# Optimization experiments

Measured on AMD Instinct MI355X. Metric: run time of the kernel, lower is better.

Reference implementation:

```python
import jax, jax.numpy as jnp
import numpy as np

B, S = 2, 1024
V, H = 32000, 1024
NH, NKV = 16, 8
HD = H // NH          # 64
L = 8
I = 4 * H             # 4096
EPS = 1e-6
THETA = 10000.0
NEG = -1e9


def setup_inputs() -> dict:
    key = jax.random.key(0)
    ks = jax.random.split(key, 12)
    std = 0.02
    f = lambda k, shape: jax.random.normal(k, shape, jnp.float32) * std
    return {
        "input_ids": jax.random.randint(ks[0], (B, S), 0, V, dtype=jnp.int32),
        "embed": f(ks[1], (V, H)),
        "Wq": f(ks[2], (L, H, NH * HD)),
        "Wk": f(ks[3], (L, H, NKV * HD)),
        "Wv": f(ks[4], (L, H, NKV * HD)),
        "Wo": f(ks[5], (L, NH * HD, H)),
        "Wg": f(ks[6], (L, H, I)),
        "Wu": f(ks[7], (L, H, I)),
        "Wd": f(ks[8], (L, I, H)),
        "ln1": jnp.ones((L, H), jnp.float32),
        "ln2": jnp.ones((L, H), jnp.float32),
        "norm_w": jnp.ones((H,), jnp.float32),
        "lm_head": f(ks[9], (H, V)),
    }


def _rmsnorm(x, w):
    var = jnp.mean(x * x, axis=-1, keepdims=True)
    return x * jax.lax.rsqrt(var + EPS) * w


def _rotate_half(x):
    x1, x2 = jnp.split(x, 2, axis=-1)
    return jnp.concatenate((-x2, x1), axis=-1)


def reference(input_ids, embed, Wq, Wk, Wv, Wo, Wg, Wu, Wd, ln1, ln2, norm_w, lm_head):
    # RoPE tables [S, HD] (freqs duplicated, matching cat((freqs, freqs)))
    inv_freq = 1.0 / (THETA ** (jnp.arange(0, HD, 2, dtype=jnp.float32) / HD))
    t = jnp.arange(S, dtype=jnp.float32)
    freqs = t[:, None] * inv_freq[None, :]
    emb = jnp.concatenate((freqs, freqs), axis=-1)
    cos = jnp.cos(emb)[None, None]  # [1,1,S,HD]
    sin = jnp.sin(emb)[None, None]
    # causal mask [S, S]
    mask = jnp.where(jnp.tril(jnp.ones((S, S), bool)), 0.0, NEG).astype(jnp.float32)

    def layer(h, p):
        wq, wk, wv, wo, wg, wu, wd, g1, g2 = p
        x = _rmsnorm(h, g1)
        q = (x @ wq).reshape(B, S, NH, HD).transpose(0, 2, 1, 3)   # [B,NH,S,HD]
        k = (x @ wk).reshape(B, S, NKV, HD).transpose(0, 2, 1, 3)  # [B,NKV,S,HD]
        v = (x @ wv).reshape(B, S, NKV, HD).transpose(0, 2, 1, 3)
        q = q * cos + _rotate_half(q) * sin
        k = k * cos + _rotate_half(k) * sin
        rep = NH // NKV
        k = jnp.repeat(k, rep, axis=1)  # GQA repeat_interleave
        v = jnp.repeat(v, rep, axis=1)
        scores = jnp.einsum("bhqd,bhkd->bhqk", q, k) / np.sqrt(HD) + mask
        probs = jax.nn.softmax(scores, axis=-1)
        o = jnp.einsum("bhqk,bhkd->bhqd", probs, v)
        o = o.transpose(0, 2, 1, 3).reshape(B, S, NH * HD)
        h = h + o @ wo
        x = _rmsnorm(h, g2)
        h = h + (jax.nn.silu(x @ wg) * (x @ wu)) @ wd
        return h, None

    h = embed[input_ids]  # [B,S,H]
    h, _ = jax.lax.scan(layer, h, (Wq, Wk, Wv, Wo, Wg, Wu, Wd, ln1, ln2))
    h = _rmsnorm(h, norm_w)
    return h @ lm_head  # logits [B,S,V]
```

## Files before the change

kernel.cpp:

```cpp
#include <hip/hip_runtime.h>


typedef unsigned short u16;
typedef __bf16  bf16x8 __attribute__((ext_vector_type(8)));
typedef unsigned short u16x8 __attribute__((ext_vector_type(8)));
typedef float   f32x4  __attribute__((ext_vector_type(4)));

#define DEV static __device__ __forceinline__

constexpr int NB  = 2;
constexpr int S   = 1024;
constexpr int NT  = NB * S;
constexpr int H   = 1024;
constexpr int NH  = 16;
constexpr int NKV = 8;
constexpr int HD  = 64;
constexpr int NL  = 8;
constexpr int FF  = 4096;
constexpr int V   = 32000;
constexpr int QKVW = 2048;

DEV float b2f(u16 x) { return __uint_as_float(((unsigned)x) << 16); }
DEV u16   f2b(float f) {
  unsigned i = __float_as_uint(f);
  return (u16)((i + 0x7fffu + ((i >> 16) & 1u)) >> 16);
}

DEV void gload16(const void* g, void* l) {
  __builtin_amdgcn_global_load_lds(
      (const __attribute__((address_space(1))) void*)g,
      (__attribute__((address_space(3))) void*)l, 16, 0, 0);
}

DEV bf16x8 ld128(const u16* p) { return *reinterpret_cast<const bf16x8*>(p); }

template <int N> DEV void waitvm() {
  if constexpr (N == 0)      asm volatile("s_waitcnt vmcnt(0)" ::: "memory");
  else if constexpr (N == 2) asm volatile("s_waitcnt vmcnt(2)" ::: "memory");
  else if constexpr (N == 3) asm volatile("s_waitcnt vmcnt(3)" ::: "memory");
  else if constexpr (N == 4) asm volatile("s_waitcnt vmcnt(4)" ::: "memory");
  else if constexpr (N == 6) asm volatile("s_waitcnt vmcnt(6)" ::: "memory");
  else                       asm volatile("s_waitcnt vmcnt(8)" ::: "memory");
}

template <int EPI>
__global__ __launch_bounds__(512, 2) void gemm256_k(
    const u16* __restrict__ A, int lda,
    const u16* __restrict__ Bt, int ldb,
    void* __restrict__ C, int ldc, int K)
{
  __shared__ __align__(16) u16 Asm[4][256 * 32];
  __shared__ __align__(16) u16 Bsm[4][256 * 32];

  const int tid  = threadIdx.x;
  const int lane = tid & 63;
  const int lrow = lane & 15;
  const int g    = lane >> 4;
  const int wid  = tid >> 6;
  const int wm   = wid >> 2, wn = wid & 3;

  int flat = blockIdx.y * gridDim.x + blockIdx.x;
  const int cpx = (gridDim.x * gridDim.y) >> 3;
  flat = (flat & 7) * cpx + (flat >> 3);
  const int bx = flat % gridDim.x;
  const int by = flat / gridDim.x;

  const int r0   = tid >> 2, pp = tid & 3;
  const int row1 = 128 + (tid >> 2);
  const int p0 = pp ^ ((r0 ^ (r0 >> 2)) & 3);
  const int p1 = pp ^ ((row1 ^ (row1 >> 2)) & 3);
  const u16* aS0 = A  + (size_t)(bx * 256 + r0)   * lda + p0 * 8;
  const u16* aS1 = A  + (size_t)(bx * 256 + row1) * lda + p1 * 8;
  const u16* bS0 = Bt + (size_t)(by * 256 + r0)   * ldb + p0 * 8;
  const u16* bS1 = Bt + (size_t)(by * 256 + row1) * ldb + p1 * 8;
  const int aB0 = tid * 16, aB1 = (512 + tid) * 16;

  int aOff[8], bOff[4];
  #pragma unroll
  for (int fm = 0; fm < 8; fm++) {
    const int r = wm * 128 + fm * 16 + lrow;
    aOff[fm] = r * 32 + (g ^ ((r ^ (r >> 2)) & 3)) * 8;
  }
  #pragma unroll
  for (int fn = 0; fn < 4; fn++) {
    const int r = wn * 64 + fn * 16 + lrow;
    bOff[fn] = r * 32 + (g ^ ((r ^ (r >> 2)) & 3)) * 8;
  }

  f32x4 acc[8][4] = {};
  const int ntk = K / 32;

  #pragma unroll
  for (int ts = 0; ts < 3; ts++) {
    const long kt = (long)ts * 32;
    gload16(aS0 + kt, (char*)Asm[ts] + aB0);
    gload16(bS0 + kt, (char*)Bsm[ts] + aB0);
    gload16(aS1 + kt, (char*)Asm[ts] + aB1);
    gload16(bS1 + kt, (char*)Bsm[ts] + aB1);
  }
  asm volatile("s_waitcnt vmcnt(8)" ::: "memory");
  __builtin_amdgcn_s_barrier();

#define KTILE(VMW, STG)                                                         \
  {                                                                             \
    const int rs = t & 3, ss = (t + 3) & 3;                                     \
    const long kt = (long)(t + 3) * 32;                                         \
    bf16x8 af[4], bf[4];                                                        \
    _Pragma("unroll") for (int i = 0; i < 4; i++) bf[i] = ld128(&Bsm[rs][bOff[i]]); \
    _Pragma("unroll") for (int i = 0; i < 4; i++) af[i] = ld128(&Asm[rs][aOff[i]]); \
    if (STG) { gload16(aS0 + kt, (char*)Asm[ss] + aB0);                         \
               gload16(bS0 + kt, (char*)Bsm[ss] + aB0); }                       \
    __builtin_amdgcn_s_barrier();                                               \
    asm volatile("s_waitcnt lgkmcnt(0)" ::: "memory");                          \
    __builtin_amdgcn_sched_barrier(0);                                          \
    __builtin_amdgcn_s_setprio(1);                                              \
    _Pragma("unroll") for (int m = 0; m < 4; m++)                               \
      _Pragma("unroll") for (int n = 0; n < 4; n++)                             \
        acc[m][n] = __builtin_amdgcn_mfma_f32_16x16x32_bf16(af[m], bf[n], acc[m][n], 0, 0, 0); \
    __builtin_amdgcn_s_setprio(0);                                              \
    __builtin_amdgcn_s_barrier();                                               \
    _Pragma("unroll") for (int i = 0; i < 4; i++) af[i] = ld128(&Asm[rs][aOff[4 + i]]); \
    if (STG) { gload16(aS1 + kt, (char*)Asm[ss] + aB1);                         \
               gload16(bS1 + kt, (char*)Bsm[ss] + aB1); }                       \
    __builtin_amdgcn_s_barrier();                                               \
    asm volatile("s_waitcnt lgkmcnt(0)" ::: "memory");                          \
    __builtin_amdgcn_sched_barrier(0);                                          \
    __builtin_amdgcn_s_setprio(1);                                              \
    _Pragma("unroll") for (int m = 0; m < 4; m++)                               \
      _Pragma("unroll") for (int n = 0; n < 4; n++)                             \
        acc[4 + m][n] = __builtin_amdgcn_mfma_f32_16x16x32_bf16(af[m], bf[n], acc[4 + m][n], 0, 0, 0); \
    __builtin_amdgcn_s_setprio(0);                                              \
    VMW;                                                                        \
    __builtin_amdgcn_sched_barrier(0);                                          \
    __builtin_amdgcn_s_barrier();                                               \
  }

  {
    int t = 0;
    for (; t < ntk - 3; ++t) KTILE(asm volatile("s_waitcnt vmcnt(8)" ::: "memory"), true);
    KTILE(asm volatile("s_waitcnt vmcnt(4)" ::: "memory"), false); ++t;
    KTILE(asm volatile("s_waitcnt vmcnt(0)" ::: "memory"), false); ++t;
    KTILE((void)0, false);
  }
#undef KTILE

  if (EPI == 2) {
    #pragma unroll
    for (int fm = 0; fm < 8; fm++) {
      #pragma unroll
      for (int fp = 0; fp < 2; fp++) {
        #pragma unroll
        for (int r = 0; r < 4; r++) {
          const size_t row = bx * 256 + wm * 128 + fm * 16 + g * 4 + r;
          const int nb = by * 256 + wn * 64 + fp * 32;
          const int oc = (nb >> 5) * 16 + lrow;
          const float gg = acc[fm][2 * fp][r];
          const float uu = acc[fm][2 * fp + 1][r];
          ((u16*)C)[row * ldc + oc] = f2b(gg / (1.f + __expf(-gg)) * uu);
        }
      }
    }
  } else {
    #pragma unroll
    for (int fm = 0; fm < 8; fm++) {
      #pragma unroll
      for (int fn = 0; fn < 4; fn++) {
        #pragma unroll
        for (int r = 0; r < 4; r++) {
          const size_t row = bx * 256 + wm * 128 + fm * 16 + g * 4 + r;
          const size_t col = by * 256 + wn * 64 + fn * 16 + lrow;
          ((float*)C)[row * ldc + col] = acc[fm][fn][r];
        }
      }
    }
  }
}

template <int BM, int BN, int WM, int WN, int EPI>
__global__ __launch_bounds__(256) void gemm_k(
    const u16* __restrict__ A, int lda,
    const u16* __restrict__ Bt, int ldb,
    void* __restrict__ C, int ldc,
    const float2* __restrict__ tab, int K)
{
  constexpr int LA = (BM * 4) / 256;
  constexpr int LB = (BN * 4) / 256;
  constexpr int LT = LA + LB;

  __shared__ __align__(16) u16 Asm[4][BM * 32];
  __shared__ __align__(16) u16 Bsm[4][BN * 32];

  const int tid  = threadIdx.x;
  const int lane = tid & 63;
  const int lrow = lane & 15;
  const int kb   = lane >> 4;
  const int w    = tid >> 6;
  const int wm   = w / WN, wn = w % WN;
  constexpr int WR = BM / WM, WC = BN / WN;
  constexpr int FM = WR / 16, FN = WC / 16;

  const u16* aS[LA];
  const u16* bS[LB];
  #pragma unroll
  for (int i = 0; i < LA; i++) {
    const int row = (i * 256 + tid) >> 2, pp = tid & 3;
    const int p = pp ^ ((row ^ (row >> 2)) & 3);
    aS[i] = A + (size_t)(blockIdx.x * BM + row) * lda + p * 8;
  }
  #pragma unroll
  for (int i = 0; i < LB; i++) {
    const int row = (i * 256 + tid) >> 2, pp = tid & 3;
    const int p = pp ^ ((row ^ (row >> 2)) & 3);
    bS[i] = Bt + (size_t)(blockIdx.y * BN + row) * ldb + p * 8;
  }

  int aOff[FM], bOff[FN];
  #pragma unroll
  for (int fm = 0; fm < FM; fm++) {
    const int r = wm * WR + fm * 16 + lrow;
    aOff[fm] = r * 32 + (kb ^ ((r ^ (r >> 2)) & 3)) * 8;
  }
  #pragma unroll
  for (int fn = 0; fn < FN; fn++) {
    const int r = wn * WC + fn * 16 + lrow;
    bOff[fn] = r * 32 + (kb ^ ((r ^ (r >> 2)) & 3)) * 8;
  }

  f32x4 acc[FM][FN] = {};
  const int ntk = K / 32;

  #pragma unroll
  for (int ts = 0; ts < 3; ts++) {
    #pragma unroll
    for (int i = 0; i < LA; i++)
      gload16(aS[i] + ts * 32, (char*)Asm[ts] + (i * 256 + tid) * 16);
    #pragma unroll
    for (int i = 0; i < LB; i++)
      gload16(bS[i] + ts * 32, (char*)Bsm[ts] + (i * 256 + tid) * 16);
  }
  waitvm<2 * LT>();
  __builtin_amdgcn_s_barrier();

#define SKTILE(VMW, STG)                                                        \
  {                                                                             \
    const int rs = t & 3, ss = (t + 3) & 3;                                     \
    const long kt = (long)(t + 3) * 32;                                         \
    bf16x8 af[FM], bf[FN];                                                      \
    _Pragma("unroll") for (int i = 0; i < FN; i++) bf[i] = ld128(&Bsm[rs][bOff[i]]); \
    _Pragma("unroll") for (int i = 0; i < FM; i++) af[i] = ld128(&Asm[rs][aOff[i]]); \
    if (STG) {                                                                  \
      _Pragma("unroll") for (int i = 0; i < LA; i++)                            \
        gload16(aS[i] + kt, (char*)Asm[ss] + (i * 256 + tid) * 16);             \
      _Pragma("unroll") for (int i = 0; i < LB; i++)                            \
        gload16(bS[i] + kt, (char*)Bsm[ss] + (i * 256 + tid) * 16);             \
    }                                                                           \
    __builtin_amdgcn_s_barrier();                                               \
    asm volatile("s_waitcnt lgkmcnt(0)" ::: "memory");                          \
    __builtin_amdgcn_sched_barrier(0);                                          \
    __builtin_amdgcn_s_setprio(1);                                              \
    _Pragma("unroll") for (int m = 0; m < FM; m++)                              \
      _Pragma("unroll") for (int n = 0; n < FN; n++)                            \
        acc[m][n] = __builtin_amdgcn_mfma_f32_16x16x32_bf16(af[m], bf[n], acc[m][n], 0, 0, 0); \
    __builtin_amdgcn_s_setprio(0);                                              \
    VMW;                                                                        \
    __builtin_amdgcn_sched_barrier(0);                                          \
    __builtin_amdgcn_s_barrier();                                               \
  }

  {
    int t = 0;
    for (; t < ntk - 3; ++t) SKTILE(waitvm<2 * LT>(), true);
    SKTILE(waitvm<LT>(), false); ++t;
    SKTILE(waitvm<0>(), false); ++t;
    SKTILE((void)0, false);
  }
#undef SKTILE

  if (EPI == 4) {
    const int colb = blockIdx.y * BN + wn * WC;
    const int head = colb >> 6;
    const float qs = (head < 16) ? 0.125f : 1.0f;
    #pragma unroll
    for (int fm = 0; fm < FM; fm++) {
      #pragma unroll
      for (int r = 0; r < 4; r++) {
        const int row = blockIdx.x * BM + wm * WR + fm * 16 + kb * 4 + r;
        if (head >= 24) {
          #pragma unroll
          for (int fn = 0; fn < FN; fn++)
            ((u16*)C)[row * ldc + colb + fn * 16 + lrow] = f2b(acc[fm][fn][r]);
        } else {
          const int s = row & (S - 1);
          #pragma unroll
          for (int fp = 0; fp < 2; fp++) {
            const int d = fp * 16 + lrow;
            const float2 cs = tab[s * 32 + d];
            const float x1 = acc[fm][fp][r];
            const float x2 = acc[fm][fp + 2][r];
            ((u16*)C)[row * ldc + colb + d]      = f2b((x1 * cs.x - x2 * cs.y) * qs);
            ((u16*)C)[row * ldc + colb + d + 32] = f2b((x2 * cs.x + x1 * cs.y) * qs);
          }
        }
      }
    }
  } else {
    #pragma unroll
    for (int fm = 0; fm < FM; fm++) {
      #pragma unroll
      for (int fn = 0; fn < FN; fn++) {
        #pragma unroll
        for (int r = 0; r < 4; r++) {
          const int row = blockIdx.x * BM + wm * WR + fm * 16 + kb * 4 + r;
          const int col = blockIdx.y * BN + wn * WC + fn * 16 + lrow;
          ((u16*)C)[row * ldc + col] = f2b(acc[fm][fn][r]);
        }
      }
    }
  }
}

__global__ __launch_bounds__(256) void transpose_k(
    const float* __restrict__ W, u16* __restrict__ WT, int K, int N, int rmode,
    size_t wstride, size_t tstride)
{
  __shared__ float t[32][33];
  const float* Wp = W + (size_t)blockIdx.z * wstride;
  u16* WTp = WT + (size_t)blockIdx.z * tstride;
  const int k0 = blockIdx.x * 32, n0 = blockIdx.y * 32;
  const int tx = threadIdx.x & 31, ty = threadIdx.x >> 5;
  #pragma unroll
  for (int i = 0; i < 32; i += 8)
    t[ty + i][tx] = Wp[(size_t)(k0 + ty + i) * N + (n0 + tx)];
  __syncthreads();
  #pragma unroll
  for (int i = 0; i < 32; i += 8) {
    const int n = n0 + ty + i;
    const int orow = (rmode == 0) ? n : ((n >> 4) * 32 + (n & 15) + ((rmode == 2) ? 16 : 0));
    WTp[(size_t)orow * K + (k0 + tx)] = f2b(t[tx][ty + i]);
  }
}

__global__ __launch_bounds__(256) void embed_k(
    const int* __restrict__ ids, const float* __restrict__ E, float* __restrict__ h)
{
  const int t = blockIdx.x;
  const int id = ids[t];
  ((float4*)(h + t * H))[threadIdx.x] = ((const float4*)(E + (size_t)id * H))[threadIdx.x];
}

__global__ __launch_bounds__(256) void rmsnorm_k(
    const float* __restrict__ h, const float* __restrict__ w, u16* __restrict__ x)
{
  const int row = blockIdx.x;
  const float4 hv = ((const float4*)(h + row * H))[threadIdx.x];
  float s = hv.x * hv.x + hv.y * hv.y + hv.z * hv.z + hv.w * hv.w;
  #pragma unroll
  for (int off = 32; off; off >>= 1) s += __shfl_xor(s, off, 64);
  __shared__ float red[4];
  if ((threadIdx.x & 63) == 0) red[threadIdx.x >> 6] = s;
  __syncthreads();
  s = red[0] + red[1] + red[2] + red[3];
  const float scale = rsqrtf(s * (1.f / H) + 1e-6f);
  const float4 wv = ((const float4*)w)[threadIdx.x];
  ushort4 ov;
  ov.x = f2b(hv.x * scale * wv.x);
  ov.y = f2b(hv.y * scale * wv.y);
  ov.z = f2b(hv.z * scale * wv.z);
  ov.w = f2b(hv.w * scale * wv.w);
  ((ushort4*)(x + row * H))[threadIdx.x] = ov;
}

__global__ __launch_bounds__(256) void addnorm_k(
    float* __restrict__ h, const u16* __restrict__ dl,
    const float* __restrict__ w, u16* __restrict__ x)
{
  const int row = blockIdx.x;
  float4 hv = ((const float4*)(h + row * H))[threadIdx.x];
  const ushort4 dv = ((const ushort4*)(dl + row * H))[threadIdx.x];
  hv.x += b2f(dv.x); hv.y += b2f(dv.y); hv.z += b2f(dv.z); hv.w += b2f(dv.w);
  ((float4*)(h + row * H))[threadIdx.x] = hv;
  float s = hv.x * hv.x + hv.y * hv.y + hv.z * hv.z + hv.w * hv.w;
  #pragma unroll
  for (int off = 32; off; off >>= 1) s += __shfl_xor(s, off, 64);
  __shared__ float red[4];
  if ((threadIdx.x & 63) == 0) red[threadIdx.x >> 6] = s;
  __syncthreads();
  s = red[0] + red[1] + red[2] + red[3];
  const float scale = rsqrtf(s * (1.f / H) + 1e-6f);
  const float4 wv = ((const float4*)w)[threadIdx.x];
  ushort4 ov;
  ov.x = f2b(hv.x * scale * wv.x);
  ov.y = f2b(hv.y * scale * wv.y);
  ov.z = f2b(hv.z * scale * wv.z);
  ov.w = f2b(hv.w * scale * wv.w);
  ((ushort4*)(x + row * H))[threadIdx.x] = ov;
}

__global__ __launch_bounds__(256) void ropetab_k(float2* __restrict__ tab)
{
  const int idx = blockIdx.x * 256 + threadIdx.x;
  const int s = idx >> 5, d = idx & 31;
  const float ang = s * powf(10000.f, -(2.f * d) / 64.f);
  float sn, cs;
  sincosf(ang, &sn, &cs);
  tab[idx] = make_float2(cs, sn);
}

__global__ __launch_bounds__(256) void fattn_k(
    const u16* __restrict__ qkv, u16* __restrict__ o)
{
  __shared__ __align__(16) u16 Ks[64 * 64];
  __shared__ __align__(16) u16 Vt[64 * 72];
  __shared__ __align__(16) u16 Pw[4][16 * 64];

  const int tid  = threadIdx.x;
  const int lane = tid & 63;
  const int lrow = lane & 15;
  const int g    = lane >> 4;
  const int w    = tid >> 6;

  const int bid = blockIdx.x;
  const int j   = bid >> 3;
  const int bh  = (bid & 7) * 4 + (j & 3);
  const int bx  = 15 - (j >> 2);
  const int b = bh >> 4, hh = bh & 15, kh = hh >> 1;
  const int q0 = bx * 64;

  bf16x8 aq[2];
  {
    const int qrow = q0 + w * 16 + lrow;
    const u16* qp = qkv + (size_t)(b * S + qrow) * QKVW + hh * 64 + g * 8;
    aq[0] = *reinterpret_cast<const bf16x8*>(qp);
    aq[1] = *reinterpret_cast<const bf16x8*>(qp + 32);
  }

  f32x4 oacc[4] = {};
  float mrow[4], lsum[4];
  #pragma unroll
  for (int r = 0; r < 4; r++) { mrow[r] = -1e30f; lsum[r] = 0.f; }

  const int nt = bx + 1;
  for (int t = 0; t < nt; t++) {
    const int kv0 = t * 64;
    __syncthreads();

    #pragma unroll
    for (int i = 0; i < 2; i++) {
      const int c = i * 256 + tid;
      const int r = c >> 3, p = c & 7;
      gload16(qkv + (size_t)(b * S + kv0 + r) * QKVW + 1024 + kh * 64 + ((p ^ (r & 7)) * 8),
              (char*)Ks + c * 16);
    }
    u16x8 vreg[2];
    #pragma unroll
    for (int i = 0; i < 2; i++) {
      const int c = i * 256 + tid;
      const int k = c >> 3, dch = c & 7;
      vreg[i] = *reinterpret_cast<const u16x8*>(
          qkv + (size_t)(b * S + kv0 + k) * QKVW + 1536 + kh * 64 + dch * 8);
    }
    #pragma unroll
    for (int i = 0; i < 2; i++) {
      const int c = i * 256 + tid;
      const int k = c >> 3, d0 = (c & 7) * 8;
      #pragma unroll
      for (int j2 = 0; j2 < 8; j2++) {
        const int d = d0 + j2;
        Vt[d * 72 + (((k >> 3) ^ (d >> 3)) * 8) + (k & 7)] = vreg[i][j2];
      }
    }
    __syncthreads();

    f32x4 sacc[4] = {};
    #pragma unroll
    for (int n = 0; n < 4; n++) {
      const int row = n * 16 + lrow;
      #pragma unroll
      for (int k2 = 0; k2 < 2; k2++) {
        const bf16x8 bk = *reinterpret_cast<const bf16x8*>(
            Ks + row * 64 + (((k2 * 4 + g) ^ (row & 7)) * 8));
        sacc[n] = __builtin_amdgcn_mfma_f32_16x16x32_bf16(aq[k2], bk, sacc[n], 0, 0, 0);
      }
    }

    float rmv[4];
    #pragma unroll
    for (int r = 0; r < 4; r++) {
      const int qglob = q0 + w * 16 + g * 4 + r;
      float rm = -1e30f;
      #pragma unroll
      for (int n = 0; n < 4; n++) {
        const int kg = kv0 + n * 16 + lrow;
        if (kg > qglob) sacc[n][r] = -1e30f;
        rm = fmaxf(rm, sacc[n][r]);
      }
      #pragma unroll
      for (int mk = 1; mk < 16; mk <<= 1) rm = fmaxf(rm, __shfl_xor(rm, mk, 64));
      rmv[r] = rm;
    }

    int need = 0;
    #pragma unroll
    for (int r = 0; r < 4; r++) need |= (rmv[r] > mrow[r] + 8.f) ? 1 : 0;
    if (__any(need)) {
      #pragma unroll
      for (int r = 0; r < 4; r++) {
        const float mnew  = fmaxf(mrow[r], rmv[r]);
        const float scale = __expf(mrow[r] - mnew);
        mrow[r] = mnew;
        lsum[r] *= scale;
        #pragma unroll
        for (int dt = 0; dt < 4; dt++) oacc[dt][r] *= scale;
      }
    }

    #pragma unroll
    for (int r = 0; r < 4; r++) {
      float rs = 0.f;
      u16 pb[4];
      #pragma unroll
      for (int n = 0; n < 4; n++) {
        const float p = __expf(sacc[n][r] - mrow[r]);
        rs += p;
        pb[n] = f2b(p);
      }
      #pragma unroll
      for (int mk = 1; mk < 16; mk <<= 1) rs += __shfl_xor(rs, mk, 64);
      lsum[r] += rs;
      const int ql = g * 4 + r;
      #pragma unroll
      for (int n = 0; n < 4; n++) {
        const int k = n * 16 + lrow;
        Pw[w][ql * 64 + (((k >> 3) ^ (ql & 7)) * 8) + (k & 7)] = pb[n];
      }
    }

    #pragma unroll
    for (int k2 = 0; k2 < 2; k2++) {
      const bf16x8 pa = *reinterpret_cast<const bf16x8*>(
          &Pw[w][lrow * 64 + (((k2 * 4 + g) ^ (lrow & 7)) * 8)]);
      #pragma unroll
      for (int dt = 0; dt < 4; dt++) {
        const int d = dt * 16 + lrow;
        const bf16x8 vb = *reinterpret_cast<const bf16x8*>(
            &Vt[d * 72 + (((k2 * 4 + g) ^ (d >> 3)) * 8)]);
        oacc[dt] = __builtin_amdgcn_mfma_f32_16x16x32_bf16(pa, vb, oacc[dt], 0, 0, 0);
      }
    }
  }

  #pragma unroll
  for (int dt = 0; dt < 4; dt++) {
    #pragma unroll
    for (int r = 0; r < 4; r++) {
      const int qrow = q0 + w * 16 + g * 4 + r;
      o[(size_t)(b * S + qrow) * H + hh * 64 + dt * 16 + lrow] =
          f2b(oacc[dt][r] / lsum[r]);
    }
  }
}

extern "C" void kernel_launch(void* const* d_in, const int* in_sizes, int n_in,
                              void* d_out, int out_size, void* d_ws, size_t ws_size,
                              hipStream_t stream)
{
  const int*   ids  = (const int*)d_in[0];
  const float* EW   = (const float*)d_in[1];
  const float* Wq   = (const float*)d_in[2];
  const float* Wk   = (const float*)d_in[3];
  const float* Wv   = (const float*)d_in[4];
  const float* Wo   = (const float*)d_in[5];
  const float* Wg   = (const float*)d_in[6];
  const float* Wu   = (const float*)d_in[7];
  const float* Wd   = (const float*)d_in[8];
  const float* ln1  = (const float*)d_in[9];
  const float* ln2  = (const float*)d_in[10];
  const float* nw   = (const float*)d_in[11];
  const float* lmw  = (const float*)d_in[12];
  float* out = (float*)d_out;

  const size_t MB = 1u << 20;
  char* ws = (char*)d_ws;
  float*  h   = (float*)(ws);
  u16*    x   = (u16*)(ws + 8 * MB);
  u16*    qkv = (u16*)(ws + 12 * MB);
  u16*    o   = (u16*)(ws + 20 * MB);
  u16*    dl  = (u16*)(ws + 24 * MB);
  u16*    ub  = (u16*)(ws + 28 * MB);
  float2* tab = (float2*)(ws + 44 * MB);
  char*   wb  = ws + 45 * MB;

  const size_t sqkv = (size_t)QKVW * H;
  const size_t swo  = (size_t)H * H;
  const size_t sgu  = (size_t)2 * FF * H;
  const size_t swd  = (size_t)H * FF;

  const bool full = ws_size >= 349 * MB;
  if (!full && ws_size < 108 * MB) return;

  u16 *wqkvT, *woT, *wguT, *wdT, *lmT;
  if (full) {
    wqkvT = (u16*)wb;
    woT   = wqkvT + NL * sqkv;
    wguT  = woT + NL * swo;
    wdT   = wguT + NL * sgu;
    lmT   = wdT + NL * swd;
  } else {
    wqkvT = (u16*)wb;
    woT   = wqkvT + sqkv;
    wguT  = woT + swo;
    wdT   = wguT + sgu;
    lmT   = (u16*)wb;
  }

  auto xpose = [&](int l0, int lz, bool dense) {
    const size_t tq = dense ? sqkv : 0, to = dense ? swo : 0;
    const size_t tg = dense ? sgu : 0,  td = dense ? swd : 0;
    transpose_k<<<dim3(H / 32, H / 32, lz), 256, 0, stream>>>(
        Wq + (size_t)l0 * H * H, wqkvT + (size_t)l0 * tq, H, H, 0, (size_t)H * H, tq);
    transpose_k<<<dim3(H / 32, 512 / 32, lz), 256, 0, stream>>>(
        Wk + (size_t)l0 * H * 512, wqkvT + (size_t)l0 * tq + (size_t)1024 * H, H, 512, 0,
        (size_t)H * 512, tq);
    transpose_k<<<dim3(H / 32, 512 / 32, lz), 256, 0, stream>>>(
        Wv + (size_t)l0 * H * 512, wqkvT + (size_t)l0 * tq + (size_t)1536 * H, H, 512, 0,
        (size_t)H * 512, tq);
    transpose_k<<<dim3(H / 32, H / 32, lz), 256, 0, stream>>>(
        Wo + (size_t)l0 * H * H, woT + (size_t)l0 * to, H, H, 0, (size_t)H * H, to);
    transpose_k<<<dim3(H / 32, FF / 32, lz), 256, 0, stream>>>(
        Wg + (size_t)l0 * H * FF, wguT + (size_t)l0 * tg, H, FF, 1, (size_t)H * FF, tg);
    transpose_k<<<dim3(H / 32, FF / 32, lz), 256, 0, stream>>>(
        Wu + (size_t)l0 * H * FF, wguT + (size_t)l0 * tg, H, FF, 2, (size_t)H * FF, tg);
    transpose_k<<<dim3(FF / 32, H / 32, lz), 256, 0, stream>>>(
        Wd + (size_t)l0 * FF * H, wdT + (size_t)l0 * td, FF, H, 0, (size_t)FF * H, td);
  };

  embed_k<<<NT, 256, 0, stream>>>(ids, EW, h);
  ropetab_k<<<(S * 32) / 256, 256, 0, stream>>>(tab);

  if (full) {
    xpose(0, NL, true);
    transpose_k<<<dim3(H / 32, V / 32, 1), 256, 0, stream>>>(lmw, lmT, H, V, 0, 0, 0);
  }

  rmsnorm_k<<<NT, 256, 0, stream>>>(h, ln1, x);

  for (int l = 0; l < NL; l++) {
    if (!full) xpose(l, 1, false);
    u16* pq = wqkvT + (full ? (size_t)l * sqkv : 0);
    u16* po = woT   + (full ? (size_t)l * swo  : 0);
    u16* pg = wguT  + (full ? (size_t)l * sgu  : 0);
    u16* pd = wdT   + (full ? (size_t)l * swd  : 0);

    gemm_k<64, 128, 2, 2, 4><<<dim3(NT / 64, QKVW / 128), 256, 0, stream>>>(
        x, H, pq, H, qkv, QKVW, tab, H);
    fattn_k<<<dim3(512), 256, 0, stream>>>(qkv, o);
    gemm_k<64, 64, 2, 2, 0><<<dim3(NT / 64, H / 64), 256, 0, stream>>>(
        o, H, po, H, dl, H, nullptr, H);
    addnorm_k<<<NT, 256, 0, stream>>>(h, dl, ln2 + l * H, x);

    gemm256_k<2><<<dim3(NT / 256, (2 * FF) / 256), 512, 0, stream>>>(
        x, H, pg, H, ub, FF, H);
    gemm_k<64, 64, 2, 2, 0><<<dim3(NT / 64, H / 64), 256, 0, stream>>>(
        ub, FF, pd, FF, dl, H, nullptr, FF);
    const float* nxt = (l + 1 < NL) ? (ln1 + (l + 1) * H) : nw;
    addnorm_k<<<NT, 256, 0, stream>>>(h, dl, nxt, x);
  }

  if (!full)
    transpose_k<<<dim3(H / 32, V / 32, 1), 256, 0, stream>>>(lmw, lmT, H, V, 0, 0, 0);
  gemm256_k<3><<<dim3(NT / 256, V / 256), 512, 0, stream>>>(
      x, H, lmT, H, out, V, H);
}
```

Baseline: 1.810 ms.

## Switch GEMM kernels from 4-stage to 2-stage LDS double buffering

Both GEMM kernels now keep two LDS stages instead of four and prefetch two k-tiles ahead, reusing the buffer just read once a barrier confirms all fragments are loaded. The 256x256 kernel also loads all eight A fragments at once and issues all 32 MFMAs in a single phase instead of two half-phases. This halves shared memory per block, which could allow more blocks per CU, and simplifies the loop. The cost is a shallower prefetch, so global memory latency is less well hidden, and the 256 kernel holds more VGPRs for A fragments.

```diff
diff --git a/kernel.cpp b/kernel.cpp
--- a/kernel.cpp
+++ b/kernel.cpp
@@ -49,8 +49,8 @@
     const u16* __restrict__ Bt, int ldb,
     void* __restrict__ C, int ldc, int K)
 {
-  __shared__ __align__(16) u16 Asm[4][256 * 32];
-  __shared__ __align__(16) u16 Bsm[4][256 * 32];
+  __shared__ __align__(16) u16 Asm[2][256 * 32];
+  __shared__ __align__(16) u16 Bsm[2][256 * 32];
 
   const int tid  = threadIdx.x;
   const int lane = tid & 63;
@@ -91,58 +91,46 @@
   const int ntk = K / 32;
 
   #pragma unroll
-  for (int ts = 0; ts < 3; ts++) {
+  for (int ts = 0; ts < 2; ts++) {
     const long kt = (long)ts * 32;
     gload16(aS0 + kt, (char*)Asm[ts] + aB0);
     gload16(bS0 + kt, (char*)Bsm[ts] + aB0);
     gload16(aS1 + kt, (char*)Asm[ts] + aB1);
     gload16(bS1 + kt, (char*)Bsm[ts] + aB1);
   }
-  asm volatile("s_waitcnt vmcnt(8)" ::: "memory");
+  waitvm<4>();
   __builtin_amdgcn_s_barrier();
 
-#define KTILE(VMW, STG)                                                         \
-  {                                                                             \
-    const int rs = t & 3, ss = (t + 3) & 3;                                     \
-    const long kt = (long)(t + 3) * 32;                                         \
-    bf16x8 af[4], bf[4];                                                        \
-    _Pragma("unroll") for (int i = 0; i < 4; i++) bf[i] = ld128(&Bsm[rs][bOff[i]]); \
-    _Pragma("unroll") for (int i = 0; i < 4; i++) af[i] = ld128(&Asm[rs][aOff[i]]); \
-    if (STG) { gload16(aS0 + kt, (char*)Asm[ss] + aB0);                         \
-               gload16(bS0 + kt, (char*)Bsm[ss] + aB0); }                       \
-    __builtin_amdgcn_s_barrier();                                               \
-    asm volatile("s_waitcnt lgkmcnt(0)" ::: "memory");                          \
-    __builtin_amdgcn_sched_barrier(0);                                          \
-    __builtin_amdgcn_s_setprio(1);                                              \
-    _Pragma("unroll") for (int m = 0; m < 4; m++)                               \
-      _Pragma("unroll") for (int n = 0; n < 4; n++)                             \
-        acc[m][n] = __builtin_amdgcn_mfma_f32_16x16x32_bf16(af[m], bf[n], acc[m][n], 0, 0, 0); \
-    __builtin_amdgcn_s_setprio(0);                                              \
-    __builtin_amdgcn_s_barrier();                                               \
-    _Pragma("unroll") for (int i = 0; i < 4; i++) af[i] = ld128(&Asm[rs][aOff[4 + i]]); \
-    if (STG) { gload16(aS1 + kt, (char*)Asm[ss] + aB1);                         \
-               gload16(bS1 + kt, (char*)Bsm[ss] + aB1); }                       \
-    __builtin_amdgcn_s_barrier();                                               \
-    asm volatile("s_waitcnt lgkmcnt(0)" ::: "memory");                          \
-    __builtin_amdgcn_sched_barrier(0);                                          \
-    __builtin_amdgcn_s_setprio(1);                                              \
-    _Pragma("unroll") for (int m = 0; m < 4; m++)                               \
-      _Pragma("unroll") for (int n = 0; n < 4; n++)                             \
-        acc[4 + m][n] = __builtin_amdgcn_mfma_f32_16x16x32_bf16(af[m], bf[n], acc[4 + m][n], 0, 0, 0); \
-    __builtin_amdgcn_s_setprio(0);                                              \
-    VMW;                                                                        \
-    __builtin_amdgcn_sched_barrier(0);                                          \
-    __builtin_amdgcn_s_barrier();                                               \
-  }
-
-  {
-    int t = 0;
-    for (; t < ntk - 3; ++t) KTILE(asm volatile("s_waitcnt vmcnt(8)" ::: "memory"), true);
-    KTILE(asm volatile("s_waitcnt vmcnt(4)" ::: "memory"), false); ++t;
-    KTILE(asm volatile("s_waitcnt vmcnt(0)" ::: "memory"), false); ++t;
-    KTILE((void)0, false);
-  }
-#undef KTILE
+  for (int t = 0; t < ntk; ++t) {
+    const int rs = t & 1;
+    bf16x8 af[8], bf[4];
+    #pragma unroll
+    for (int i = 0; i < 4; i++) bf[i] = ld128(&Bsm[rs][bOff[i]]);
+    #pragma unroll
+    for (int i = 0; i < 8; i++) af[i] = ld128(&Asm[rs][aOff[i]]);
+    asm volatile("s_waitcnt lgkmcnt(0)" ::: "memory");
+    __builtin_amdgcn_sched_barrier(0);
+    __builtin_amdgcn_s_barrier();
+    if (t + 2 < ntk) {
+      const long kt = (long)(t + 2) * 32;
+      gload16(aS0 + kt, (char*)Asm[rs] + aB0);
+      gload16(bS0 + kt, (char*)Bsm[rs] + aB0);
+      gload16(aS1 + kt, (char*)Asm[rs] + aB1);
+      gload16(bS1 + kt, (char*)Bsm[rs] + aB1);
+    }
+    __builtin_amdgcn_s_setprio(1);
+    #pragma unroll
+    for (int m = 0; m < 8; m++) {
+      #pragma unroll
+      for (int n = 0; n < 4; n++)
+        acc[m][n] = __builtin_amdgcn_mfma_f32_16x16x32_bf16(af[m], bf[n], acc[m][n], 0, 0, 0);
+    }
+    __builtin_amdgcn_s_setprio(0);
+    if (t + 2 < ntk)      waitvm<4>();
+    else if (t + 1 < ntk) waitvm<0>();
+    __builtin_amdgcn_sched_barrier(0);
+    __builtin_amdgcn_s_barrier();
+  }
 
   if (EPI == 2) {
     #pragma unroll
@@ -187,8 +175,8 @@
   constexpr int LB = (BN * 4) / 256;
   constexpr int LT = LA + LB;
 
-  __shared__ __align__(16) u16 Asm[4][BM * 32];
-  __shared__ __align__(16) u16 Bsm[4][BN * 32];
+  __shared__ __align__(16) u16 Asm[2][BM * 32];
+  __shared__ __align__(16) u16 Bsm[2][BN * 32];
 
   const int tid  = threadIdx.x;
   const int lane = tid & 63;
@@ -230,7 +218,7 @@
   const int ntk = K / 32;
 
   #pragma unroll
-  for (int ts = 0; ts < 3; ts++) {
+  for (int ts = 0; ts < 2; ts++) {
     #pragma unroll
     for (int i = 0; i < LA; i++)
       gload16(aS[i] + ts * 32, (char*)Asm[ts] + (i * 256 + tid) * 16);
@@ -238,43 +226,41 @@
     for (int i = 0; i < LB; i++)
       gload16(bS[i] + ts * 32, (char*)Bsm[ts] + (i * 256 + tid) * 16);
   }
-  waitvm<2 * LT>();
+  waitvm<LT>();
   __builtin_amdgcn_s_barrier();
 
-#define SKTILE(VMW, STG)                                                        \
-  {                                                                             \
-    const int rs = t & 3, ss = (t + 3) & 3;                                     \
-    const long kt = (long)(t + 3) * 32;                                         \
-    bf16x8 af[FM], bf[FN];                                                      \
-    _Pragma("unroll") for (int i = 0; i < FN; i++) bf[i] = ld128(&Bsm[rs][bOff[i]]); \
-    _Pragma("unroll") for (int i = 0; i < FM; i++) af[i] = ld128(&Asm[rs][aOff[i]]); \
-    if (STG) {                                                                  \
-      _Pragma("unroll") for (int i = 0; i < LA; i++)                            \
-        gload16(aS[i] + kt, (char*)Asm[ss] + (i * 256 + tid) * 16);             \
-      _Pragma("unroll") for (int i = 0; i < LB; i++)                            \
-        gload16(bS[i] + kt, (char*)Bsm[ss] + (i * 256 + tid) * 16);             \
-    }                                                                           \
-    __builtin_amdgcn_s_barrier();                                               \
-    asm volatile("s_waitcnt lgkmcnt(0)" ::: "memory");                          \
-    __builtin_amdgcn_sched_barrier(0);                                          \
-    __builtin_amdgcn_s_setprio(1);                                              \
-    _Pragma("unroll") for (int m = 0; m < FM; m++)                              \
-      _Pragma("unroll") for (int n = 0; n < FN; n++)                            \
-        acc[m][n] = __builtin_amdgcn_mfma_f32_16x16x32_bf16(af[m], bf[n], acc[m][n], 0, 0, 0); \
-    __builtin_amdgcn_s_setprio(0);                                              \
-    VMW;                                                                        \
-    __builtin_amdgcn_sched_barrier(0);                                          \
-    __builtin_amdgcn_s_barrier();                                               \
-  }
-
-  {
-    int t = 0;
-    for (; t < ntk - 3; ++t) SKTILE(waitvm<2 * LT>(), true);
-    SKTILE(waitvm<LT>(), false); ++t;
-    SKTILE(waitvm<0>(), false); ++t;
-    SKTILE((void)0, false);
-  }
-#undef SKTILE
+  for (int t = 0; t < ntk; ++t) {
+    const int rs = t & 1;
+    bf16x8 af[FM], bf[FN];
+    #pragma unroll
+    for (int i = 0; i < FN; i++) bf[i] = ld128(&Bsm[rs][bOff[i]]);
+    #pragma unroll
+    for (int i = 0; i < FM; i++) af[i] = ld128(&Asm[rs][aOff[i]]);
+    asm volatile("s_waitcnt lgkmcnt(0)" ::: "memory");
+    __builtin_amdgcn_sched_barrier(0);
+    __builtin_amdgcn_s_barrier();
+    if (t + 2 < ntk) {
+      const long kt = (long)(t + 2) * 32;
+      #pragma unroll
+      for (int i = 0; i < LA; i++)
+        gload16(aS[i] + kt, (char*)Asm[rs] + (i * 256 + tid) * 16);
+      #pragma unroll
+      for (int i = 0; i < LB; i++)
+        gload16(bS[i] + kt, (char*)Bsm[rs] + (i * 256 + tid) * 16);
+    }
+    __builtin_amdgcn_s_setprio(1);
+    #pragma unroll
+    for (int m = 0; m < FM; m++) {
+      #pragma unroll
+      for (int n = 0; n < FN; n++)
+        acc[m][n] = __builtin_amdgcn_mfma_f32_16x16x32_bf16(af[m], bf[n], acc[m][n], 0, 0, 0);
+    }
+    __builtin_amdgcn_s_setprio(0);
+    if (t + 2 < ntk)      waitvm<LT>();
+    else if (t + 1 < ntk) waitvm<0>();
+    __builtin_amdgcn_sched_barrier(0);
+    __builtin_amdgcn_s_barrier();
+  }
 
   if (EPI == 4) {
     const int colb = blockIdx.y * BN + wn * WC;
```

Result: slower. 1.970 ms (+8.8%).

## Load GEMM A operand directly into registers, staging only B through LDS

Applied to the files above, without the earlier changes.

The A tile is no longer staged in shared memory. Each wave loads its own A fragments straight from global memory into registers with a one-tile register double buffer (even/odd). Only B goes through LDS via a 4-stage buffer with a 2-tile lookahead. This halves LDS traffic and footprint and removes one barrier pair per k-tile. In exchange it raises register pressure and issues uncoalesced 16-byte global loads of A that are replicated across the 4 N-waves, with tighter vmcnt bookkeeping that could stall or be wrong if the counts are off.

```diff
diff --git a/kernel.cpp b/kernel.cpp
--- a/kernel.cpp
+++ b/kernel.cpp
@@ -35,12 +35,14 @@
 DEV bf16x8 ld128(const u16* p) { return *reinterpret_cast<const bf16x8*>(p); }
 
 template <int N> DEV void waitvm() {
-  if constexpr (N == 0)      asm volatile("s_waitcnt vmcnt(0)" ::: "memory");
-  else if constexpr (N == 2) asm volatile("s_waitcnt vmcnt(2)" ::: "memory");
-  else if constexpr (N == 3) asm volatile("s_waitcnt vmcnt(3)" ::: "memory");
-  else if constexpr (N == 4) asm volatile("s_waitcnt vmcnt(4)" ::: "memory");
-  else if constexpr (N == 6) asm volatile("s_waitcnt vmcnt(6)" ::: "memory");
-  else                       asm volatile("s_waitcnt vmcnt(8)" ::: "memory");
+  if constexpr (N == 0)       asm volatile("s_waitcnt vmcnt(0)" ::: "memory");
+  else if constexpr (N == 2)  asm volatile("s_waitcnt vmcnt(2)" ::: "memory");
+  else if constexpr (N == 3)  asm volatile("s_waitcnt vmcnt(3)" ::: "memory");
+  else if constexpr (N == 4)  asm volatile("s_waitcnt vmcnt(4)" ::: "memory");
+  else if constexpr (N == 6)  asm volatile("s_waitcnt vmcnt(6)" ::: "memory");
+  else if constexpr (N == 8)  asm volatile("s_waitcnt vmcnt(8)" ::: "memory");
+  else if constexpr (N == 10) asm volatile("s_waitcnt vmcnt(10)" ::: "memory");
+  else                        asm volatile("s_waitcnt vmcnt(12)" ::: "memory");
 }
 
 template <int EPI>
@@ -49,7 +51,6 @@
     const u16* __restrict__ Bt, int ldb,
     void* __restrict__ C, int ldc, int K)
 {
-  __shared__ __align__(16) u16 Asm[4][256 * 32];
   __shared__ __align__(16) u16 Bsm[4][256 * 32];
 
   const int tid  = threadIdx.x;
@@ -69,80 +70,76 @@
   const int row1 = 128 + (tid >> 2);
   const int p0 = pp ^ ((r0 ^ (r0 >> 2)) & 3);
   const int p1 = pp ^ ((row1 ^ (row1 >> 2)) & 3);
-  const u16* aS0 = A  + (size_t)(bx * 256 + r0)   * lda + p0 * 8;
-  const u16* aS1 = A  + (size_t)(bx * 256 + row1) * lda + p1 * 8;
   const u16* bS0 = Bt + (size_t)(by * 256 + r0)   * ldb + p0 * 8;
   const u16* bS1 = Bt + (size_t)(by * 256 + row1) * ldb + p1 * 8;
-  const int aB0 = tid * 16, aB1 = (512 + tid) * 16;
-
-  int aOff[8], bOff[4];
-  #pragma unroll
-  for (int fm = 0; fm < 8; fm++) {
-    const int r = wm * 128 + fm * 16 + lrow;
-    aOff[fm] = r * 32 + (g ^ ((r ^ (r >> 2)) & 3)) * 8;
-  }
+  const int lB0 = tid * 16, lB1 = (512 + tid) * 16;
+
+  int bOff[4];
   #pragma unroll
   for (int fn = 0; fn < 4; fn++) {
     const int r = wn * 64 + fn * 16 + lrow;
     bOff[fn] = r * 32 + (g ^ ((r ^ (r >> 2)) & 3)) * 8;
   }
 
+  const u16* aP[8];
+  #pragma unroll
+  for (int fm = 0; fm < 8; fm++) {
+    const int r = bx * 256 + wm * 128 + fm * 16 + lrow;
+    aP[fm] = A + (size_t)r * lda + g * 8;
+  }
+
   f32x4 acc[8][4] = {};
   const int ntk = K / 32;
 
-  #pragma unroll
-  for (int ts = 0; ts < 3; ts++) {
-    const long kt = (long)ts * 32;
-    gload16(aS0 + kt, (char*)Asm[ts] + aB0);
-    gload16(bS0 + kt, (char*)Bsm[ts] + aB0);
-    gload16(aS1 + kt, (char*)Asm[ts] + aB1);
-    gload16(bS1 + kt, (char*)Bsm[ts] + aB1);
-  }
-  asm volatile("s_waitcnt vmcnt(8)" ::: "memory");
+  gload16(bS0 + 0,  (char*)Bsm[0] + lB0);
+  gload16(bS1 + 0,  (char*)Bsm[0] + lB1);
+  gload16(bS0 + 32, (char*)Bsm[1] + lB0);
+  gload16(bS1 + 32, (char*)Bsm[1] + lB1);
+  __builtin_amdgcn_sched_barrier(0);
+  bf16x8 aE[8], aO[8];
+  #pragma unroll
+  for (int i = 0; i < 8; i++) aE[i] = ld128(aP[i]);
+  __builtin_amdgcn_sched_barrier(0);
+  gload16(bS0 + 64, (char*)Bsm[2] + lB0);
+  gload16(bS1 + 64, (char*)Bsm[2] + lB1);
+  waitvm<12>();
   __builtin_amdgcn_s_barrier();
 
-#define KTILE(VMW, STG)                                                         \
+#define GBODY(T, ACUR, ANXT, LOADA, STGB, VMW)                                  \
   {                                                                             \
-    const int rs = t & 3, ss = (t + 3) & 3;                                     \
-    const long kt = (long)(t + 3) * 32;                                         \
-    bf16x8 af[4], bf[4];                                                        \
-    _Pragma("unroll") for (int i = 0; i < 4; i++) bf[i] = ld128(&Bsm[rs][bOff[i]]); \
-    _Pragma("unroll") for (int i = 0; i < 4; i++) af[i] = ld128(&Asm[rs][aOff[i]]); \
-    if (STG) { gload16(aS0 + kt, (char*)Asm[ss] + aB0);                         \
-               gload16(bS0 + kt, (char*)Bsm[ss] + aB0); }                       \
-    __builtin_amdgcn_s_barrier();                                               \
+    const int t_ = (T);                                                         \
+    bf16x8 bf[4];                                                               \
+    _Pragma("unroll") for (int i = 0; i < 4; i++)                               \
+      bf[i] = ld128(&Bsm[t_ & 3][bOff[i]]);                                     \
+    if (LOADA) {                                                                \
+      _Pragma("unroll") for (int i = 0; i < 8; i++)                             \
+        ANXT[i] = ld128(aP[i] + (long)(t_ + 1) * 32);                           \
+    }                                                                           \
+    if (STGB) {                                                                 \
+      const long kt = (long)(t_ + 2) * 32;                                      \
+      gload16(bS0 + kt, (char*)Bsm[(t_ + 2) & 3] + lB0);                        \
+      gload16(bS1 + kt, (char*)Bsm[(t_ + 2) & 3] + lB1);                        \
+    }                                                                           \
     asm volatile("s_waitcnt lgkmcnt(0)" ::: "memory");                          \
     __builtin_amdgcn_sched_barrier(0);                                          \
+    __builtin_amdgcn_s_barrier();                                               \
     __builtin_amdgcn_s_setprio(1);                                              \
-    _Pragma("unroll") for (int m = 0; m < 4; m++)                               \
+    _Pragma("unroll") for (int m = 0; m < 8; m++)                               \
       _Pragma("unroll") for (int n = 0; n < 4; n++)                             \
-        acc[m][n] = __builtin_amdgcn_mfma_f32_16x16x32_bf16(af[m], bf[n], acc[m][n], 0, 0, 0); \
-    __builtin_amdgcn_s_setprio(0);                                              \
-    __builtin_amdgcn_s_barrier();                                               \
-    _Pragma("unroll") for (int i = 0; i < 4; i++) af[i] = ld128(&Asm[rs][aOff[4 + i]]); \
-    if (STG) { gload16(aS1 + kt, (char*)Asm[ss] + aB1);                         \
-               gload16(bS1 + kt, (char*)Bsm[ss] + aB1); }                       \
-    __builtin_amdgcn_s_barrier();                                               \
-    asm volatile("s_waitcnt lgkmcnt(0)" ::: "memory");                          \
-    __builtin_amdgcn_sched_barrier(0);                                          \
-    __builtin_amdgcn_s_setprio(1);                                              \
-    _Pragma("unroll") for (int m = 0; m < 4; m++)                               \
-      _Pragma("unroll") for (int n = 0; n < 4; n++)                             \
-        acc[4 + m][n] = __builtin_amdgcn_mfma_f32_16x16x32_bf16(af[m], bf[n], acc[4 + m][n], 0, 0, 0); \
+        acc[m][n] = __builtin_amdgcn_mfma_f32_16x16x32_bf16(ACUR[m], bf[n], acc[m][n], 0, 0, 0); \
     __builtin_amdgcn_s_setprio(0);                                              \
     VMW;                                                                        \
     __builtin_amdgcn_sched_barrier(0);                                          \
     __builtin_amdgcn_s_barrier();                                               \
   }
 
-  {
-    int t = 0;
-    for (; t < ntk - 3; ++t) KTILE(asm volatile("s_waitcnt vmcnt(8)" ::: "memory"), true);
-    KTILE(asm volatile("s_waitcnt vmcnt(4)" ::: "memory"), false); ++t;
-    KTILE(asm volatile("s_waitcnt vmcnt(0)" ::: "memory"), false); ++t;
-    KTILE((void)0, false);
-  }
-#undef KTILE
+  for (int t = 0; t + 2 < ntk; t += 2) {
+    GBODY(t,     aE, aO, true, true,              waitvm<10>());
+    GBODY(t + 1, aO, aE, true, (t + 3 < ntk),     waitvm<10>());
+  }
+  GBODY(ntk - 2, aE, aO, true,  false, waitvm<8>());
+  GBODY(ntk - 1, aO, aE, false, false, (void)0);
+#undef GBODY
 
   if (EPI == 2) {
     #pragma unroll
```

Measured after the change: 2.222 ms. +22.8%, slower.
